# Optimization experiments

Measured on AMD Instinct MI355X. Metric: run time of the kernel, lower is better.

## Reference

```python
import jax, jax.numpy as jnp
import numpy as np

N = 50000       # nodes
E = 500000      # edges
F_IN = 64       # input feature dim
F_OUT = 64      # hidden/output dim
K = 3           # diffusion filter order
C = F_IN + F_OUT  # concat dim seen by each DConv


def _xavier(k, shape):
    fan_in, fan_out = shape[-2], shape[-1]
    lim = float(np.sqrt(6.0 / (fan_in + fan_out)))
    return jax.random.uniform(k, shape, jnp.float32, -lim, lim)


def setup_inputs() -> dict:
    key = jax.random.key(0)
    ks = jax.random.split(key, 8)
    X = jax.random.normal(ks[0], (N, F_IN), jnp.float32)
    H = jax.random.normal(ks[1], (N, F_OUT), jnp.float32)
    # ring edges guarantee every node has in-degree >= 1 and out-degree >= 1
    base = jnp.arange(N, dtype=jnp.int32)
    row = jnp.concatenate([base, jax.random.randint(ks[2], (E - N,), 0, N, jnp.int32)])
    col = jnp.concatenate([jnp.roll(base, 1), jax.random.randint(ks[3], (E - N,), 0, N, jnp.int32)])
    edge_index = jnp.stack([row, col])  # [2, E]
    W_z = _xavier(ks[4], (2, K, C, F_OUT))
    W_r = _xavier(ks[5], (2, K, C, F_OUT))
    W_h = _xavier(ks[6], (2, K, C, F_OUT))
    b = jnp.zeros((F_OUT,), jnp.float32)
    return {"X": X, "edge_index": edge_index, "H": H,
            "W_z": W_z, "b_z": b, "W_r": W_r, "b_r": b, "W_h": W_h, "b_h": b}


def _dconv(Xc, row, col, norm_out, norm_in, W, b):
    # PyG propagate: gather source (row) features, scale by edge norm, scatter-add to target (col)
    def prop(x, norm):
        return jax.ops.segment_sum(norm[:, None] * x[row], col, num_segments=N)
    Tx_0 = Xc
    Hout = Xc @ (W[0, 0] + W[1, 0])
    Tx_1_o = prop(Xc, norm_out)
    Tx_1_i = prop(Xc, norm_in)
    Hout = Hout + Tx_1_o @ W[0, 1] + Tx_1_i @ W[1, 1]
    for k in range(2, K):
        Tx_2_o = 2.0 * prop(Tx_1_o, norm_out) - Tx_0
        Tx_2_i = 2.0 * prop(Tx_1_i, norm_in) - Tx_0
        Hout = Hout + Tx_2_o @ W[0, k] + Tx_2_i @ W[1, k]
        # faithful to original: Tx_1 is never reassigned, so Tx_0 stays Xc
        Tx_0, Tx_1_o, Tx_1_i = Xc, Tx_2_o, Tx_2_i
    return Hout + b


def reference(X, edge_index, H, W_z, b_z, W_r, b_r, W_h, b_h):
    row, col = edge_index[0], edge_index[1]
    deg_out = jnp.zeros((N,), jnp.float32).at[row].add(1.0)
    deg_in = jnp.zeros((N,), jnp.float32).at[col].add(1.0)
    norm_out = (1.0 / deg_out)[row]
    norm_in = (1.0 / deg_in)[row]
    XH = jnp.concatenate([X, H], axis=1)
    Z = jax.nn.sigmoid(_dconv(XH, row, col, norm_out, norm_in, W_z, b_z))
    R = jax.nn.sigmoid(_dconv(XH, row, col, norm_out, norm_in, W_r, b_r))
    XHR = jnp.concatenate([X, H * R], axis=1)
    H_tilde = jnp.tanh(_dconv(XHR, row, col, norm_out, norm_in, W_h, b_h))
    H_new = Z * H + (1.0 - Z) * H_tilde
    # NaN infill with mean of non-NaN entries (faithful to original)
    mask = jnp.isnan(H_new)
    H_new = jnp.where(mask, jnp.nanmean(H_new), H_new)
    return H_new
```

## Files before the change

### kernel.cpp

```cpp
#include <hip/hip_runtime.h>
#include <hip/hip_bf16.h>
#include <math.h>

#define N_NODES 50000
#define N_EDGES 500000
#define C_DIM 128
#define N_TILES 3125

#define CSR_BLOCKS 489
#define CONCAT_BLOCKS 3125
#define PACK_BLOCKS 480

typedef __attribute__((ext_vector_type(8))) short bf8;
typedef __attribute__((ext_vector_type(4))) float f32x4;
typedef __attribute__((ext_vector_type(2))) float f32x2;

__device__ __forceinline__ float bflo(unsigned u) { return __uint_as_float(u << 16); }
__device__ __forceinline__ float bfhi(unsigned u) { return __uint_as_float(u & 0xffff0000u); }
__device__ __forceinline__ unsigned short f2bfu(float f) {
    __hip_bfloat16 h = __float2bfloat16(f);
    unsigned short u;
    __builtin_memcpy(&u, &h, 2);
    return u;
}
__device__ __forceinline__ unsigned packbf(float a, float b) {
    return ((unsigned)f2bfu(b) << 16) | f2bfu(a);
}


__global__ void count_deg(const int* __restrict__ row, const int* __restrict__ col,
                          int* __restrict__ dout, int* __restrict__ din, int e) {
    int i = blockIdx.x * blockDim.x + threadIdx.x;
    if (i >= e) return;
    atomicAdd(&dout[row[i]], 1);
    atomicAdd(&din[col[i]], 1);
}

__global__ void scan_block(const int* __restrict__ counts, int* __restrict__ excl,
                           int* __restrict__ blocksums, int n) {
    __shared__ int tmp[1024];
    int tid = threadIdx.x;
    int gid = blockIdx.x * 1024 + tid;
    int v = (gid < n) ? counts[gid] : 0;
    tmp[tid] = v;
    __syncthreads();
    for (int off = 1; off < 1024; off <<= 1) {
        int t = (tid >= off) ? tmp[tid - off] : 0;
        __syncthreads();
        tmp[tid] += t;
        __syncthreads();
    }
    int incl = tmp[tid];
    if (gid < n) excl[gid] = incl - v;
    if (tid == 1023) blocksums[blockIdx.x] = incl;
}

__global__ void scan_sums(int* __restrict__ blocksums, int nb) {
    __shared__ int tmp[64];
    int tid = threadIdx.x;
    int v = (tid < nb) ? blocksums[tid] : 0;
    tmp[tid] = v;
    __syncthreads();
    for (int off = 1; off < 64; off <<= 1) {
        int t = (tid >= off) ? tmp[tid - off] : 0;
        __syncthreads();
        tmp[tid] += t;
        __syncthreads();
    }
    if (tid < nb) blocksums[tid] = tmp[tid] - v;
}

__global__ void scan_add(int* __restrict__ rowptr, const int* __restrict__ blocksums,
                         int* __restrict__ cursor, const int* __restrict__ dout,
                         const int* __restrict__ din, float2* __restrict__ winv,
                         int n, int e_total) {
    int gid = blockIdx.x * blockDim.x + threadIdx.x;
    if (gid < n) {
        int v = rowptr[gid] + blocksums[gid >> 10];
        rowptr[gid] = v;
        cursor[gid] = v;
        winv[gid] = make_float2(1.0f / (float)dout[gid], 1.0f / (float)din[gid]);
    }
    if (gid == n) rowptr[n] = e_total;
}

__device__ __forceinline__ float wraw(const float* W, int d, int kk, int k, int j) {
    return W[((d * 3 + kk) * 128 + k) * 64 + j];
}

__device__ __forceinline__ float zr_val(const float* Wz, const float* Wr, int k, int nn) {
    const float* W = (nn < 64) ? Wz : Wr;
    int j = nn & 63;
    if (k < 128) return wraw(W, 0, 0, k, j) + wraw(W, 1, 0, k, j);
    int k2 = k - 128;
    int kk = (k2 >= 256) ? 2 : 1;
    int k3 = k2 & 255;
    int p = k3 >> 2, sub = k3 & 3;
    return wraw(W, sub >> 1, kk, 2 * p + (sub & 1), j);
}

__device__ __forceinline__ float h_val(const float* Wh, int k, int j) {
    if (k < 64) return wraw(Wh, 0, 0, k, j) + wraw(Wh, 1, 0, k, j);
    if (k < 320) {
        int k2 = k - 64;
        int kk = (k2 >= 128) ? 2 : 1;
        int k3 = k2 & 127;
        int p = k3 >> 2, sub = k3 & 3;
        return wraw(Wh, sub >> 1, kk, 2 * p + (sub & 1), j);
    }
    if (k < 384) return wraw(Wh, 0, 0, 64 + (k - 320), j) + wraw(Wh, 1, 0, 64 + (k - 320), j);
    int k2 = k - 384;
    int kk = (k2 >= 128) ? 2 : 1;
    int k3 = k2 & 127;
    int p = k3 >> 2, sub = k3 & 3;
    return wraw(Wh, sub >> 1, kk, 64 + 2 * p + (sub & 1), j);
}

__global__ void fused_prep(const int* __restrict__ row, const int* __restrict__ col,
                           int* __restrict__ cursor,
                           int* __restrict__ csr_src,
                           const float* __restrict__ X, const float* __restrict__ Hm,
                           unsigned short* __restrict__ XH, unsigned short* __restrict__ XHp,
                           const float* Wz, const float* Wr,
                           const float* Wh,
                           unsigned short* __restrict__ Wzrf, unsigned short* __restrict__ Whf,
                           int n, int e) {
    int b = blockIdx.x;
    if (b < CSR_BLOCKS) {
        int base = b * 1024 + threadIdx.x;
#pragma unroll
        for (int k = 0; k < 4; ++k) {
            int i = base + k * 256;
            if (i < e) {
                int r = row[i], c = col[i];
                int pos = atomicAdd(&cursor[c], 1);
                csr_src[pos] = r;
            }
        }
    } else if (b < CSR_BLOCKS + CONCAT_BLOCKS) {
        int t = (b - CSR_BLOCKS) * 256 + threadIdx.x;
        int node = t >> 4, p = t & 15;
        const float* src = (p < 8) ? (X + (size_t)node * 64 + 8 * p)
                                   : (Hm + (size_t)node * 64 + 8 * (p - 8));
        float4 v0 = *(const float4*)src;
        float4 v1 = *(const float4*)(src + 4);
        uint4 o;
        o.x = packbf(v0.x, v0.y); o.y = packbf(v0.z, v0.w);
        o.z = packbf(v1.x, v1.y); o.w = packbf(v1.z, v1.w);
        *(uint4*)(XH + (size_t)node * 128 + 8 * p) = o;
        int tile = node >> 4, lr = node & 15, ck = p >> 2, q = p & 3;
        *(uint4*)(XHp + (((size_t)tile * 4 + ck) * 64 + q * 16 + lr) * 8) = o;
    } else {
        int i = (b - CSR_BLOCKS - CONCAT_BLOCKS) * 256 + threadIdx.x;
        if (i < 20 * 8 * 64 * 8) {
            int j = i & 7, lane = (i >> 3) & 63, nt = (i >> 9) & 7, ks = i >> 12;
            int k = ks * 32 + (lane >> 4) * 8 + j;
            int nn = nt * 16 + (lane & 15);
            Wzrf[i] = f2bfu(zr_val(Wz, Wr, k, nn));
        } else if (i < 20 * 8 * 64 * 8 + 20 * 4 * 64 * 8) {
            int i2 = i - 20 * 8 * 64 * 8;
            int j = i2 & 7, lane = (i2 >> 3) & 63, nt = (i2 >> 9) & 3, ks = i2 >> 11;
            int k = ks * 32 + (lane >> 4) * 8 + j;
            int nn = nt * 16 + (lane & 15);
            Whf[i2] = f2bfu(h_val(Wh, k, nn));
        }
    }
}


__global__ void prop1_128(const unsigned short* __restrict__ S,
                          const int* __restrict__ rowptr, const int* __restrict__ src,
                          const float2* __restrict__ winv,
                          unsigned char* __restrict__ P18, unsigned short* __restrict__ P1p,
                          int n) {
    int tid = blockIdx.x * blockDim.x + threadIdx.x;
    int lane = tid & 63;
    int node = ((tid >> 6) << 1) + (lane >> 5);
    int p = lane & 31;
    if (node >= n) return;
    int beg = rowptr[node], end = rowptr[node + 1];
    float ao0 = 0.f, ao1 = 0.f, ao2 = 0.f, ao3 = 0.f;
    float ai0 = 0.f, ai1 = 0.f, ai2 = 0.f, ai3 = 0.f;
    int j = beg;
#define P1STEP(s_, w_) {                                                     \
        uint2 u = *(const uint2*)(S + (size_t)(s_) * 128 + 4 * p);           \
        float c0 = bflo(u.x), c1 = bfhi(u.x), c2 = bflo(u.y), c3 = bfhi(u.y);\
        ao0 = fmaf(w_.x, c0, ao0); ao1 = fmaf(w_.x, c1, ao1);                \
        ao2 = fmaf(w_.x, c2, ao2); ao3 = fmaf(w_.x, c3, ao3);                \
        ai0 = fmaf(w_.y, c0, ai0); ai1 = fmaf(w_.y, c1, ai1);                \
        ai2 = fmaf(w_.y, c2, ai2); ai3 = fmaf(w_.y, c3, ai3); }
    for (; j + 8 <= end; j += 8) {
        int s0 = src[j], s1 = src[j + 1], s2 = src[j + 2], s3 = src[j + 3];
        int s4 = src[j + 4], s5 = src[j + 5], s6 = src[j + 6], s7 = src[j + 7];
        float2 w0 = winv[s0], w1 = winv[s1], w2 = winv[s2], w3 = winv[s3];
        float2 w4 = winv[s4], w5 = winv[s5], w6 = winv[s6], w7 = winv[s7];
        P1STEP(s0, w0); P1STEP(s1, w1); P1STEP(s2, w2); P1STEP(s3, w3);
        P1STEP(s4, w4); P1STEP(s5, w5); P1STEP(s6, w6); P1STEP(s7, w7);
    }
    for (; j + 4 <= end; j += 4) {
        int s0 = src[j], s1 = src[j + 1], s2 = src[j + 2], s3 = src[j + 3];
        float2 w0 = winv[s0], w1 = winv[s1], w2 = winv[s2], w3 = winv[s3];
        P1STEP(s0, w0); P1STEP(s1, w1); P1STEP(s2, w2); P1STEP(s3, w3);
    }
    for (; j < end; ++j) {
        int s = src[j]; float2 wv = winv[s];
        P1STEP(s, wv);
    }
#undef P1STEP
    unsigned wa = (unsigned)__builtin_amdgcn_cvt_pk_fp8_f32(ao0, ao1, 0, false);
    wa = (unsigned)__builtin_amdgcn_cvt_pk_fp8_f32(ai0, ai1, wa, true);
    unsigned wb = (unsigned)__builtin_amdgcn_cvt_pk_fp8_f32(ao2, ao3, 0, false);
    wb = (unsigned)__builtin_amdgcn_cvt_pk_fp8_f32(ai2, ai3, wb, true);
    uint2 o8; o8.x = wa; o8.y = wb;
    *(uint2*)(P18 + (size_t)node * 256 + 8 * p) = o8;
    uint4 o;
    o.x = packbf(ao0, ao1); o.y = packbf(ai0, ai1);
    o.z = packbf(ao2, ao3); o.w = packbf(ai2, ai3);
    int tile = node >> 4, lr = node & 15, ck = p >> 2, q = p & 3;
    *(uint4*)(P1p + (((size_t)tile * 8 + ck) * 64 + q * 16 + lr) * 8) = o;
}

__global__ void prop2_128(const unsigned char* __restrict__ P18,
                          const unsigned short* __restrict__ Xc,
                          const int* __restrict__ rowptr, const int* __restrict__ src,
                          const float2* __restrict__ winv,
                          unsigned short* __restrict__ P2p, int n) {
    int tid = blockIdx.x * blockDim.x + threadIdx.x;
    int lane = tid & 63;
    int node = ((tid >> 6) << 1) + (lane >> 5);
    int p = lane & 31;
    if (node >= n) return;
    int beg = rowptr[node], end = rowptr[node + 1];
    float oa = 0.f, ob = 0.f, oc = 0.f, od = 0.f;
    float ia = 0.f, ib = 0.f, ic = 0.f, id = 0.f;
    int j = beg;
#define P2STEP(s_, w_) {                                                     \
        uint2 v = *(const uint2*)(P18 + (size_t)(s_) * 256 + 8 * p);         \
        f32x2 f0 = __builtin_amdgcn_cvt_pk_f32_fp8(v.x, false);              \
        f32x2 f1 = __builtin_amdgcn_cvt_pk_f32_fp8(v.x, true);               \
        f32x2 f2 = __builtin_amdgcn_cvt_pk_f32_fp8(v.y, false);              \
        f32x2 f3 = __builtin_amdgcn_cvt_pk_f32_fp8(v.y, true);               \
        oa = fmaf(w_.x, f0[0], oa); ob = fmaf(w_.x, f0[1], ob);              \
        ia = fmaf(w_.y, f1[0], ia); ib = fmaf(w_.y, f1[1], ib);              \
        oc = fmaf(w_.x, f2[0], oc); od = fmaf(w_.x, f2[1], od);              \
        ic = fmaf(w_.y, f3[0], ic); id = fmaf(w_.y, f3[1], id); }
    for (; j + 8 <= end; j += 8) {
        int s0 = src[j], s1 = src[j + 1], s2 = src[j + 2], s3 = src[j + 3];
        int s4 = src[j + 4], s5 = src[j + 5], s6 = src[j + 6], s7 = src[j + 7];
        float2 w0 = winv[s0], w1 = winv[s1], w2 = winv[s2], w3 = winv[s3];
        float2 w4 = winv[s4], w5 = winv[s5], w6 = winv[s6], w7 = winv[s7];
        P2STEP(s0, w0); P2STEP(s1, w1); P2STEP(s2, w2); P2STEP(s3, w3);
        P2STEP(s4, w4); P2STEP(s5, w5); P2STEP(s6, w6); P2STEP(s7, w7);
    }
    for (; j + 4 <= end; j += 4) {
        int s0 = src[j], s1 = src[j + 1], s2 = src[j + 2], s3 = src[j + 3];
        float2 w0 = winv[s0], w1 = winv[s1], w2 = winv[s2], w3 = winv[s3];
        P2STEP(s0, w0); P2STEP(s1, w1); P2STEP(s2, w2); P2STEP(s3, w3);
    }
    for (; j < end; ++j) {
        int s = src[j]; float2 wv = winv[s];
        P2STEP(s, wv);
    }
#undef P2STEP
    uint2 ux = *(const uint2*)(Xc + (size_t)node * 128 + 4 * p);
    float xa = bflo(ux.x), xb = bfhi(ux.x), xc = bflo(ux.y), xd = bfhi(ux.y);
    uint4 o;
    o.x = packbf(2.f * oa - xa, 2.f * ob - xb);
    o.y = packbf(2.f * ia - xa, 2.f * ib - xb);
    o.z = packbf(2.f * oc - xc, 2.f * od - xd);
    o.w = packbf(2.f * ic - xc, 2.f * id - xd);
    int tile = node >> 4, lr = node & 15, ck = p >> 2, q = p & 3;
    *(uint4*)(P2p + (((size_t)tile * 8 + ck) * 64 + q * 16 + lr) * 8) = o;
}

__global__ void prop1_64(const unsigned short* __restrict__ HR,
                         const int* __restrict__ rowptr, const int* __restrict__ src,
                         const float2* __restrict__ winv,
                         unsigned char* __restrict__ Q18, unsigned short* __restrict__ Q1p,
                         int n) {
    int tid = blockIdx.x * blockDim.x + threadIdx.x;
    int lane = tid & 63;
    int node = ((tid >> 6) << 2) + (lane >> 4);
    int p = lane & 15;
    if (node >= n) return;
    int beg = rowptr[node], end = rowptr[node + 1];
    float ao0 = 0.f, ao1 = 0.f, ao2 = 0.f, ao3 = 0.f;
    float ai0 = 0.f, ai1 = 0.f, ai2 = 0.f, ai3 = 0.f;
    int j = beg;
#define Q1STEP(s_, w_) {                                                     \
        uint2 u = *(const uint2*)(HR + (size_t)(s_) * 64 + 4 * p);           \
        float c0 = bflo(u.x), c1 = bfhi(u.x), c2 = bflo(u.y), c3 = bfhi(u.y);\
        ao0 = fmaf(w_.x, c0, ao0); ao1 = fmaf(w_.x, c1, ao1);                \
        ao2 = fmaf(w_.x, c2, ao2); ao3 = fmaf(w_.x, c3, ao3);                \
        ai0 = fmaf(w_.y, c0, ai0); ai1 = fmaf(w_.y, c1, ai1);                \
        ai2 = fmaf(w_.y, c2, ai2); ai3 = fmaf(w_.y, c3, ai3); }
    for (; j + 8 <= end; j += 8) {
        int s0 = src[j], s1 = src[j + 1], s2 = src[j + 2], s3 = src[j + 3];
        int s4 = src[j + 4], s5 = src[j + 5], s6 = src[j + 6], s7 = src[j + 7];
        float2 w0 = winv[s0], w1 = winv[s1], w2 = winv[s2], w3 = winv[s3];
        float2 w4 = winv[s4], w5 = winv[s5], w6 = winv[s6], w7 = winv[s7];
        Q1STEP(s0, w0); Q1STEP(s1, w1); Q1STEP(s2, w2); Q1STEP(s3, w3);
        Q1STEP(s4, w4); Q1STEP(s5, w5); Q1STEP(s6, w6); Q1STEP(s7, w7);
    }
    for (; j + 4 <= end; j += 4) {
        int s0 = src[j], s1 = src[j + 1], s2 = src[j + 2], s3 = src[j + 3];
        float2 w0 = winv[s0], w1 = winv[s1], w2 = winv[s2], w3 = winv[s3];
        Q1STEP(s0, w0); Q1STEP(s1, w1); Q1STEP(s2, w2); Q1STEP(s3, w3);
    }
    for (; j < end; ++j) {
        int s = src[j]; float2 wv = winv[s];
        Q1STEP(s, wv);
    }
#undef Q1STEP
    unsigned wa = (unsigned)__builtin_amdgcn_cvt_pk_fp8_f32(ao0, ao1, 0, false);
    wa = (unsigned)__builtin_amdgcn_cvt_pk_fp8_f32(ai0, ai1, wa, true);
    unsigned wb = (unsigned)__builtin_amdgcn_cvt_pk_fp8_f32(ao2, ao3, 0, false);
    wb = (unsigned)__builtin_amdgcn_cvt_pk_fp8_f32(ai2, ai3, wb, true);
    uint2 o8; o8.x = wa; o8.y = wb;
    *(uint2*)(Q18 + (size_t)node * 128 + 8 * p) = o8;
    uint4 o;
    o.x = packbf(ao0, ao1); o.y = packbf(ai0, ai1);
    o.z = packbf(ao2, ao3); o.w = packbf(ai2, ai3);
    int tile = node >> 4, lr = node & 15, ck = p >> 2, q = p & 3;
    *(uint4*)(Q1p + (((size_t)tile * 4 + ck) * 64 + q * 16 + lr) * 8) = o;
}

__global__ void prop2_64(const unsigned char* __restrict__ Q18,
                         const unsigned short* __restrict__ HR,
                         const int* __restrict__ rowptr, const int* __restrict__ src,
                         const float2* __restrict__ winv,
                         unsigned short* __restrict__ Q2p, int n) {
    int tid = blockIdx.x * blockDim.x + threadIdx.x;
    int lane = tid & 63;
    int node = ((tid >> 6) << 2) + (lane >> 4);
    int p = lane & 15;
    if (node >= n) return;
    int beg = rowptr[node], end = rowptr[node + 1];
    float oa = 0.f, ob = 0.f, oc = 0.f, od = 0.f;
    float ia = 0.f, ib = 0.f, ic = 0.f, id = 0.f;
    int j = beg;
#define Q2STEP(s_, w_) {                                                     \
        uint2 v = *(const uint2*)(Q18 + (size_t)(s_) * 128 + 8 * p);         \
        f32x2 f0 = __builtin_amdgcn_cvt_pk_f32_fp8(v.x, false);              \
        f32x2 f1 = __builtin_amdgcn_cvt_pk_f32_fp8(v.x, true);               \
        f32x2 f2 = __builtin_amdgcn_cvt_pk_f32_fp8(v.y, false);              \
        f32x2 f3 = __builtin_amdgcn_cvt_pk_f32_fp8(v.y, true);               \
        oa = fmaf(w_.x, f0[0], oa); ob = fmaf(w_.x, f0[1], ob);              \
        ia = fmaf(w_.y, f1[0], ia); ib = fmaf(w_.y, f1[1], ib);              \
        oc = fmaf(w_.x, f2[0], oc); od = fmaf(w_.x, f2[1], od);              \
        ic = fmaf(w_.y, f3[0], ic); id = fmaf(w_.y, f3[1], id); }
    for (; j + 8 <= end; j += 8) {
        int s0 = src[j], s1 = src[j + 1], s2 = src[j + 2], s3 = src[j + 3];
        int s4 = src[j + 4], s5 = src[j + 5], s6 = src[j + 6], s7 = src[j + 7];
        float2 w0 = winv[s0], w1 = winv[s1], w2 = winv[s2], w3 = winv[s3];
        float2 w4 = winv[s4], w5 = winv[s5], w6 = winv[s6], w7 = winv[s7];
        Q2STEP(s0, w0); Q2STEP(s1, w1); Q2STEP(s2, w2); Q2STEP(s3, w3);
        Q2STEP(s4, w4); Q2STEP(s5, w5); Q2STEP(s6, w6); Q2STEP(s7, w7);
    }
    for (; j + 4 <= end; j += 4) {
        int s0 = src[j], s1 = src[j + 1], s2 = src[j + 2], s3 = src[j + 3];
        float2 w0 = winv[s0], w1 = winv[s1], w2 = winv[s2], w3 = winv[s3];
        Q2STEP(s0, w0); Q2STEP(s1, w1); Q2STEP(s2, w2); Q2STEP(s3, w3);
    }
    for (; j < end; ++j) {
        int s = src[j]; float2 wv = winv[s];
        Q2STEP(s, wv);
    }
#undef Q2STEP
    uint2 ux = *(const uint2*)(HR + (size_t)node * 64 + 4 * p);
    float xa = bflo(ux.x), xb = bfhi(ux.x), xc = bflo(ux.y), xd = bfhi(ux.y);
    uint4 o;
    o.x = packbf(2.f * oa - xa, 2.f * ob - xb);
    o.y = packbf(2.f * ia - xa, 2.f * ib - xb);
    o.z = packbf(2.f * oc - xc, 2.f * od - xd);
    o.w = packbf(2.f * ic - xc, 2.f * id - xd);
    int tile = node >> 4, lr = node & 15, ck = p >> 2, q = p & 3;
    *(uint4*)(Q2p + (((size_t)tile * 4 + ck) * 64 + q * 16 + lr) * 8) = o;
}


__global__ __launch_bounds__(256) void gemm_zr_mfma(
    const unsigned short* __restrict__ XHp, const unsigned short* __restrict__ P1p,
    const unsigned short* __restrict__ P2p,
    const unsigned short* __restrict__ Wf, const float* bz,
    const float* br, const float* __restrict__ H,
    float* __restrict__ Zf, unsigned short* __restrict__ HR, int n) {
    int tid = threadIdx.x;
    int lane = tid & 63;
    int ngrp = tid >> 6;
    int rowbase = blockIdx.x * 32;
    int lr = lane & 15, quad = lane >> 4;

    int tiles[2];
#pragma unroll
    for (int mt = 0; mt < 2; ++mt) {
        int t = (rowbase >> 4) + mt;
        tiles[mt] = (t > N_TILES - 1) ? N_TILES - 1 : t;
    }

    auto LDB = [&](int ks, int nt) {
        return *(const bf8*)(Wf + (((size_t)ks * 8 + ngrp * 2 + nt) * 64 + lane) * 8);
    };
    auto LDA = [&](int ks, int mt) {
        const unsigned short* T = (ks < 4) ? XHp : (ks < 12) ? P1p : P2p;
        int ck = (ks < 4) ? ks : (ks < 12) ? ks - 4 : ks - 12;
        int nck = (ks < 4) ? 4 : 8;
        return *(const bf8*)(T + (((size_t)tiles[mt] * nck + ck) * 64 + lane) * 8);
    };

    f32x4 zero = {0.f, 0.f, 0.f, 0.f};
    f32x4 acc[2][2];
#pragma unroll
    for (int a = 0; a < 2; ++a)
#pragma unroll
        for (int b = 0; b < 2; ++b) acc[a][b] = zero;

    bf8 a0 = LDA(0, 0), a1 = LDA(0, 1), b0 = LDB(0, 0), b1 = LDB(0, 1);
#pragma unroll
    for (int ks = 0; ks < 20; ++ks) {
        bf8 na0, na1, nb0, nb1;
        if (ks < 19) {
            na0 = LDA(ks + 1, 0); na1 = LDA(ks + 1, 1);
            nb0 = LDB(ks + 1, 0); nb1 = LDB(ks + 1, 1);
        }
        acc[0][0] = __builtin_amdgcn_mfma_f32_16x16x32_bf16(a0, b0, acc[0][0], 0, 0, 0);
        acc[0][1] = __builtin_amdgcn_mfma_f32_16x16x32_bf16(a0, b1, acc[0][1], 0, 0, 0);
        acc[1][0] = __builtin_amdgcn_mfma_f32_16x16x32_bf16(a1, b0, acc[1][0], 0, 0, 0);
        acc[1][1] = __builtin_amdgcn_mfma_f32_16x16x32_bf16(a1, b1, acc[1][1], 0, 0, 0);
        if (ks < 19) { a0 = na0; a1 = na1; b0 = nb0; b1 = nb1; }
    }
#pragma unroll
    for (int mt = 0; mt < 2; ++mt)
#pragma unroll
        for (int reg = 0; reg < 4; ++reg) {
            int r = rowbase + mt * 16 + quad * 4 + reg;
            if (r >= n) continue;
#pragma unroll
            for (int nt = 0; nt < 2; ++nt) {
                int cidx = ngrp * 32 + nt * 16 + lr;
                float bias = (cidx < 64) ? bz[cidx] : br[cidx - 64];
                float v = acc[mt][nt][reg] + bias;
                float s = 1.f / (1.f + expf(-v));
                if (cidx < 64) {
                    Zf[(size_t)r * 64 + cidx] = s;
                } else {
                    int c2 = cidx - 64;
                    HR[(size_t)r * 64 + c2] = f2bfu(H[(size_t)r * 64 + c2] * s);
                }
            }
        }
}

__global__ __launch_bounds__(256) void gemm_h_mfma(
    const unsigned short* __restrict__ XHp, const unsigned short* __restrict__ P1p,
    const unsigned short* __restrict__ P2p, const unsigned short* __restrict__ HR,
    const unsigned short* __restrict__ Q1p, const unsigned short* __restrict__ Q2p,
    const unsigned short* __restrict__ Wf, const float* bh,
    const float* __restrict__ Zf, const float* __restrict__ H,
    float* __restrict__ out, int n) {
    int tid = threadIdx.x;
    int lane = tid & 63;
    int wid = tid >> 6;
    int mh = wid & 1, ngrp = wid >> 1;
    int rowbase = blockIdx.x * 32 + mh * 16;
    int lr = lane & 15, quad = lane >> 4;

    int t = rowbase >> 4;
    int tile = (t > N_TILES - 1) ? N_TILES - 1 : t;
    int rh = rowbase + lr;
    if (rh >= n) rh = n - 1;
    const unsigned short* hrp = HR + (size_t)rh * 64 + quad * 8;

    auto LDB = [&](int ks, int nt) {
        return *(const bf8*)(Wf + (((size_t)ks * 4 + ngrp * 2 + nt) * 64 + lane) * 8);
    };
    auto LDA = [&](int ks) {
        if (ks == 10 || ks == 11) {
            return *(const bf8*)(hrp + (ks - 10) * 32);
        }
        const unsigned short* T = (ks < 2) ? XHp : (ks < 6) ? P1p :
                                  (ks < 10) ? P2p : (ks < 16) ? Q1p : Q2p;
        int ck = (ks < 2) ? ks : (ks < 6) ? ks - 2 : (ks < 10) ? ks - 6 :
                 (ks < 16) ? ks - 12 : ks - 16;
        int nck = (ks < 2) ? 4 : (ks < 10) ? 8 : 4;
        return *(const bf8*)(T + (((size_t)tile * nck + ck) * 64 + lane) * 8);
    };

    f32x4 zero = {0.f, 0.f, 0.f, 0.f};
    f32x4 acc[2];
    acc[0] = zero; acc[1] = zero;

    bf8 a0 = LDA(0), b0 = LDB(0, 0), b1 = LDB(0, 1);
#pragma unroll
    for (int ks = 0; ks < 20; ++ks) {
        bf8 na0, nb0, nb1;
        if (ks < 19) {
            na0 = LDA(ks + 1); nb0 = LDB(ks + 1, 0); nb1 = LDB(ks + 1, 1);
        }
        acc[0] = __builtin_amdgcn_mfma_f32_16x16x32_bf16(a0, b0, acc[0], 0, 0, 0);
        acc[1] = __builtin_amdgcn_mfma_f32_16x16x32_bf16(a0, b1, acc[1], 0, 0, 0);
        if (ks < 19) { a0 = na0; b0 = nb0; b1 = nb1; }
    }
#pragma unroll
    for (int reg = 0; reg < 4; ++reg) {
        int r = rowbase + quad * 4 + reg;
        if (r >= n) continue;
#pragma unroll
        for (int nt = 0; nt < 2; ++nt) {
            int cidx = ngrp * 32 + nt * 16 + lr;
            float ht = tanhf(acc[nt][reg] + bh[cidx]);
            float z = Zf[(size_t)r * 64 + cidx];
            float h_old = H[(size_t)r * 64 + cidx];
            out[(size_t)r * 64 + cidx] = z * h_old + (1.f - z) * ht;
        }
    }
}


static inline size_t rup(size_t x) { return (x + 63) & ~(size_t)63; }

extern "C" void kernel_launch(void* const* d_in, const int* in_sizes, int n_in,
                              void* d_out, int out_size, void* d_ws, size_t ws_size,
                              hipStream_t stream) {
    const float* X  = (const float*)d_in[0];
    const int*   EI = (const int*)d_in[1];
    const float* H  = (const float*)d_in[2];
    const float* Wz = (const float*)d_in[3];
    const float* bz = (const float*)d_in[4];
    const float* Wr = (const float*)d_in[5];
    const float* br = (const float*)d_in[6];
    const float* Wh = (const float*)d_in[7];
    const float* bh = (const float*)d_in[8];
    float* out = (float*)d_out;

    const int* row = EI;
    const int* col = EI + N_EDGES;

    char* ws = (char*)d_ws;
    size_t off = 0;
    auto carve = [&](size_t bytes) { void* p = ws + off; off += rup(bytes); return p; };

    int*   deg_out   = (int*)carve(N_NODES * 4);
    int*   deg_in    = (int*)carve(N_NODES * 4);
    int*   rowptr    = (int*)carve((N_NODES + 1) * 4);
    int*   cursor    = (int*)carve(N_NODES * 4);
    int*   blocksums = (int*)carve(64 * 4);
    float2* winv     = (float2*)carve(N_NODES * 8);
    int*   csr_src   = (int*)carve(N_EDGES * 4);
    unsigned short* XH  = (unsigned short*)carve((size_t)N_NODES * 128 * 2);
    unsigned char*  Pscr = (unsigned char*)carve((size_t)N_NODES * 256 + (size_t)N_TILES * 4 * 512 * 2);
    unsigned short* XHp = (unsigned short*)carve((size_t)N_TILES * 4 * 512 * 2);
    unsigned short* P1p = (unsigned short*)carve((size_t)N_TILES * 8 * 512 * 2);
    unsigned short* P2p = (unsigned short*)carve((size_t)N_TILES * 8 * 512 * 2);
    unsigned short* HR  = (unsigned short*)carve((size_t)N_NODES * 64 * 2);
    float* Zf           = (float*)carve((size_t)N_NODES * 64 * 4);
    unsigned short* Wzrf = (unsigned short*)carve(20 * 8 * 64 * 8 * 2);
    unsigned short* Whf  = (unsigned short*)carve(20 * 4 * 64 * 8 * 2);

    unsigned char*  P18 = Pscr;
    unsigned char*  Q18 = (unsigned char*)XH;
    unsigned short* Q1p = (unsigned short*)Pscr;
    unsigned short* Q2p = (unsigned short*)(Pscr + (size_t)N_NODES * 256);

    hipMemsetAsync(deg_out, 0, rup(N_NODES * 4) + rup(N_NODES * 4), stream);
    count_deg<<<(N_EDGES + 255) / 256, 256, 0, stream>>>(row, col, deg_out, deg_in, N_EDGES);

    int nblk = (N_NODES + 1023) / 1024;
    scan_block<<<nblk, 1024, 0, stream>>>(deg_in, rowptr, blocksums, N_NODES);
    scan_sums<<<1, 64, 0, stream>>>(blocksums, nblk);
    scan_add<<<(N_NODES + 1 + 255) / 256, 256, 0, stream>>>(rowptr, blocksums, cursor,
                                                            deg_out, deg_in, winv, N_NODES, N_EDGES);

    fused_prep<<<CSR_BLOCKS + CONCAT_BLOCKS + PACK_BLOCKS, 256, 0, stream>>>(
        row, col, cursor, csr_src,
        X, H, XH, XHp, Wz, Wr, Wh, Wzrf, Whf, N_NODES, N_EDGES);

    int blocks_p128 = (((N_NODES + 1) / 2) * 64 + 255) / 256;
    prop1_128<<<blocks_p128, 256, 0, stream>>>(XH, rowptr, csr_src, winv, P18, P1p, N_NODES);
    prop2_128<<<blocks_p128, 256, 0, stream>>>(P18, XH, rowptr, csr_src, winv, P2p, N_NODES);

    int zr_blocks = (N_NODES + 31) / 32;
    gemm_zr_mfma<<<zr_blocks, 256, 0, stream>>>(XHp, P1p, P2p, Wzrf, bz, br, H, Zf, HR, N_NODES);

    int blocks_p64 = (((N_NODES + 3) / 4) * 64 + 255) / 256;
    prop1_64<<<blocks_p64, 256, 0, stream>>>(HR, rowptr, csr_src, winv, Q18, Q1p, N_NODES);
    prop2_64<<<blocks_p64, 256, 0, stream>>>(Q18, HR, rowptr, csr_src, winv, Q2p, N_NODES);

    int h_blocks = (N_NODES + 31) / 32;
    gemm_h_mfma<<<h_blocks, 256, 0, stream>>>(XHp, P1p, P2p, HR, Q1p, Q2p,
                                              Whf, bh, Zf, H, out, N_NODES);
}
```

Baseline: 326.3 us.

## Split propagation kernels into feature slices across blocks with 8 lanes per node

The four SpMM propagation kernels now give each node 8 lanes that cover a 32-feature slice (8 lanes × 4 features). The feature dimension is split across 4 blocks (128-wide) or 2 blocks (64-wide), and each block handles 32 nodes. Each wave now covers 8 nodes instead of 2 or 4, which spreads degree imbalance and raises memory-level parallelism on the gathers. Each feature-slice block handles its nodes' 32 consecutive features, so the gather working set per pass is narrower and may hit the L2 better. The cost is that rowptr, src and winv are now read redundantly by every slice block, and each gathered row access is only 64 bytes wide.

```diff
diff --git a/kernel.cpp b/kernel.cpp
--- a/kernel.cpp
+++ b/kernel.cpp
@@ -10,6 +10,8 @@
 #define CSR_BLOCKS 489
 #define CONCAT_BLOCKS 3125
 #define PACK_BLOCKS 480
+
+#define PROP_CHUNKS 1563
 
 typedef __attribute__((ext_vector_type(8))) short bf8;
 typedef __attribute__((ext_vector_type(4))) float f32x4;
@@ -173,10 +175,12 @@
                           const float2* __restrict__ winv,
                           unsigned char* __restrict__ P18, unsigned short* __restrict__ P1p,
                           int n) {
-    int tid = blockIdx.x * blockDim.x + threadIdx.x;
+    int b = blockIdx.x;
+    int slice = b & 3, chunk = b >> 2;
+    int tid = threadIdx.x;
     int lane = tid & 63;
-    int node = ((tid >> 6) << 1) + (lane >> 5);
-    int p = lane & 31;
+    int node = chunk * 32 + ((tid >> 6) << 3) + (lane >> 3);
+    int p = slice * 8 + (lane & 7);
     if (node >= n) return;
     int beg = rowptr[node], end = rowptr[node + 1];
     float ao0 = 0.f, ao1 = 0.f, ao2 = 0.f, ao3 = 0.f;
@@ -225,10 +229,12 @@
                           const int* __restrict__ rowptr, const int* __restrict__ src,
                           const float2* __restrict__ winv,
                           unsigned short* __restrict__ P2p, int n) {
-    int tid = blockIdx.x * blockDim.x + threadIdx.x;
+    int b = blockIdx.x;
+    int slice = b & 3, chunk = b >> 2;
+    int tid = threadIdx.x;
     int lane = tid & 63;
-    int node = ((tid >> 6) << 1) + (lane >> 5);
-    int p = lane & 31;
+    int node = chunk * 32 + ((tid >> 6) << 3) + (lane >> 3);
+    int p = slice * 8 + (lane & 7);
     if (node >= n) return;
     int beg = rowptr[node], end = rowptr[node + 1];
     float oa = 0.f, ob = 0.f, oc = 0.f, od = 0.f;
@@ -278,10 +284,12 @@
                          const float2* __restrict__ winv,
                          unsigned char* __restrict__ Q18, unsigned short* __restrict__ Q1p,
                          int n) {
-    int tid = blockIdx.x * blockDim.x + threadIdx.x;
+    int b = blockIdx.x;
+    int slice = b & 1, chunk = b >> 1;
+    int tid = threadIdx.x;
     int lane = tid & 63;
-    int node = ((tid >> 6) << 2) + (lane >> 4);
-    int p = lane & 15;
+    int node = chunk * 32 + ((tid >> 6) << 3) + (lane >> 3);
+    int p = slice * 8 + (lane & 7);
     if (node >= n) return;
     int beg = rowptr[node], end = rowptr[node + 1];
     float ao0 = 0.f, ao1 = 0.f, ao2 = 0.f, ao3 = 0.f;
@@ -330,10 +338,12 @@
                          const int* __restrict__ rowptr, const int* __restrict__ src,
                          const float2* __restrict__ winv,
                          unsigned short* __restrict__ Q2p, int n) {
-    int tid = blockIdx.x * blockDim.x + threadIdx.x;
+    int b = blockIdx.x;
+    int slice = b & 1, chunk = b >> 1;
+    int tid = threadIdx.x;
     int lane = tid & 63;
-    int node = ((tid >> 6) << 2) + (lane >> 4);
-    int p = lane & 15;
+    int node = chunk * 32 + ((tid >> 6) << 3) + (lane >> 3);
+    int p = slice * 8 + (lane & 7);
     if (node >= n) return;
     int beg = rowptr[node], end = rowptr[node + 1];
     float oa = 0.f, ob = 0.f, oc = 0.f, od = 0.f;
@@ -575,16 +585,14 @@
         row, col, cursor, csr_src,
         X, H, XH, XHp, Wz, Wr, Wh, Wzrf, Whf, N_NODES, N_EDGES);
 
-    int blocks_p128 = (((N_NODES + 1) / 2) * 64 + 255) / 256;
-    prop1_128<<<blocks_p128, 256, 0, stream>>>(XH, rowptr, csr_src, winv, P18, P1p, N_NODES);
-    prop2_128<<<blocks_p128, 256, 0, stream>>>(P18, XH, rowptr, csr_src, winv, P2p, N_NODES);
+    prop1_128<<<4 * PROP_CHUNKS, 256, 0, stream>>>(XH, rowptr, csr_src, winv, P18, P1p, N_NODES);
+    prop2_128<<<4 * PROP_CHUNKS, 256, 0, stream>>>(P18, XH, rowptr, csr_src, winv, P2p, N_NODES);
 
     int zr_blocks = (N_NODES + 31) / 32;
     gemm_zr_mfma<<<zr_blocks, 256, 0, stream>>>(XHp, P1p, P2p, Wzrf, bz, br, H, Zf, HR, N_NODES);
 
-    int blocks_p64 = (((N_NODES + 3) / 4) * 64 + 255) / 256;
-    prop1_64<<<blocks_p64, 256, 0, stream>>>(HR, rowptr, csr_src, winv, Q18, Q1p, N_NODES);
-    prop2_64<<<blocks_p64, 256, 0, stream>>>(Q18, HR, rowptr, csr_src, winv, Q2p, N_NODES);
+    prop1_64<<<2 * PROP_CHUNKS, 256, 0, stream>>>(HR, rowptr, csr_src, winv, Q18, Q1p, N_NODES);
+    prop2_64<<<2 * PROP_CHUNKS, 256, 0, stream>>>(Q18, HR, rowptr, csr_src, winv, Q2p, N_NODES);
 
     int h_blocks = (N_NODES + 31) / 32;
     gemm_h_mfma<<<h_blocks, 256, 0, stream>>>(XHp, P1p, P2p, HR, Q1p, Q2p,
```

Result: slower. 341.9 us (+4.8%).
